# Kernel tuning notes

Measured on AMD Instinct MI355X. Metric: run time of the kernel, lower is better.

## Reference

```python
import jax, jax.numpy as jnp
import numpy as np

D_MODEL = 1024
D_FFN = 2048
N_EXPERTS = 8
TOP_K = 2
B, S = 2, 2048
LN_EPS = 1e-5


def setup_inputs() -> dict:
    key = jax.random.key(0)
    ks = jax.random.split(key, 6)
    scale = 0.02
    x = jax.random.normal(ks[0], (B, S, D_MODEL), dtype=jnp.float32)
    w_router = jax.random.normal(ks[1], (N_EXPERTS, D_MODEL), dtype=jnp.float32) * scale
    w_gate = jax.random.normal(ks[2], (N_EXPERTS, D_FFN, D_MODEL), dtype=jnp.float32) * scale
    w_up = jax.random.normal(ks[3], (N_EXPERTS, D_FFN, D_MODEL), dtype=jnp.float32) * scale
    w_down = jax.random.normal(ks[4], (N_EXPERTS, D_MODEL, D_FFN), dtype=jnp.float32) * scale
    ln_gamma = jnp.ones((D_MODEL,), dtype=jnp.float32)
    ln_beta = jnp.zeros((D_MODEL,), dtype=jnp.float32)
    return {"x": x, "w_router": w_router, "w_gate": w_gate, "w_up": w_up,
            "w_down": w_down, "ln_gamma": ln_gamma, "ln_beta": ln_beta}


def reference(x, w_router, w_gate, w_up, w_down, ln_gamma, ln_beta):
    # Router: top-k logits, softmax over selected k (matches MoERouter)
    logits = jnp.einsum('bsd,ed->bse', x, w_router)            # [B,S,E]
    top_vals, top_idx = jax.lax.top_k(logits, TOP_K)           # [B,S,k]
    rw = jax.nn.softmax(top_vals, axis=-1)                     # [B,S,k]

    # Dense per-expert SwiGLU over ALL tokens (faithful to the looped original:
    # sum over k of mask*weight*expert(x) == gather of per-expert outputs).
    gate = jnp.einsum('bsd,efd->ebsf', x, w_gate)              # [E,B,S,F]
    up = jnp.einsum('bsd,efd->ebsf', x, w_up)                  # [E,B,S,F]
    h = jax.nn.silu(gate) * up                                 # SwiGLU hidden
    y = jnp.einsum('ebsf,edf->bsed', h, w_down)                # [B,S,E,D]

    # Gather the k selected experts per token and combine with routing weights
    sel = jnp.take_along_axis(y, top_idx[..., None], axis=2)   # [B,S,k,D]
    out = jnp.sum(rw[..., None] * sel, axis=2)                 # [B,S,D]

    # LayerNorm (eps=1e-5, elementwise affine)
    mu = jnp.mean(out, axis=-1, keepdims=True)
    var = jnp.mean(jnp.square(out - mu), axis=-1, keepdims=True)
    out = (out - mu) * jax.lax.rsqrt(var + LN_EPS)
    return out * ln_gamma + ln_beta
```

## Files before the change

kernel.cpp:

```cpp
#include <hip/hip_runtime.h>


#define D_MODEL 1024
#define D_FFN   2048
#define N_EXP   8
#define TOKENS  4096
#define LISTCAP 4096
#define ROWS_PAD 8320
#define W_ELEM  16777216u

typedef __bf16 bf16x8 __attribute__((ext_vector_type(8)));
typedef float  f32x4  __attribute__((ext_vector_type(4)));

__device__ __forceinline__ ushort f2bf(float f) {
  union { float f; unsigned u; } v; v.f = f;
  unsigned u = v.u;
  u += 0x7fffu + ((u >> 16) & 1u);
  return (ushort)(u >> 16);
}
__device__ __forceinline__ float bf2f(ushort h) {
  union { unsigned u; float f; } v; v.u = ((unsigned)h) << 16; return v.f;
}
__device__ __forceinline__ void gl2lds16(const ushort* g, ushort* l) {
  __builtin_amdgcn_global_load_lds(
      (const __attribute__((address_space(1))) unsigned int*)g,
      (__attribute__((address_space(3))) unsigned int*)l, 16, 0, 0);
}


__global__ __launch_bounds__(64) void router3_kernel(
    const float* __restrict__ x, const float* __restrict__ wr,
    ushort* __restrict__ xb, int* __restrict__ counts,
    int* __restrict__ tok_list, int* __restrict__ slots, float* __restrict__ wts)
{
  const int token = blockIdx.x;
  const int lane  = threadIdx.x;
  const float* xr = x + (size_t)token * D_MODEL + lane * 16;

  float xv[16];
  #pragma unroll
  for (int j = 0; j < 16; ++j) xv[j] = xr[j];

  ushort* xbr = xb + (size_t)token * D_MODEL + lane * 16;
  #pragma unroll
  for (int half = 0; half < 2; ++half) {
    ushort u8[8];
    #pragma unroll
    for (int j = 0; j < 8; ++j) u8[j] = f2bf(xv[half * 8 + j]);
    *(uint4*)(xbr + half * 8) = *(uint4*)u8;
  }

  float logit[N_EXP];
  #pragma unroll
  for (int e = 0; e < N_EXP; ++e) {
    const float* w = wr + e * D_MODEL + lane * 16;
    float p = 0.f;
    #pragma unroll
    for (int j = 0; j < 16; ++j) p += xv[j] * w[j];
    #pragma unroll
    for (int o = 32; o > 0; o >>= 1) p += __shfl_xor(p, o, 64);
    logit[e] = p;
  }

  if (lane == 0) {
    float v0 = -1e30f, v1 = -1e30f; int i0 = 0, i1 = 0;
    #pragma unroll
    for (int e = 0; e < N_EXP; ++e) {
      float v = logit[e];
      if (v > v0)      { v1 = v0; i1 = i0; v0 = v; i0 = e; }
      else if (v > v1) { v1 = v; i1 = e; }
    }
    float t  = expf(v1 - v0);
    float w0 = 1.f / (1.f + t);
    float w1 = t   / (1.f + t);
    int p0 = atomicAdd(&counts[i0], 1);
    tok_list[i0 * LISTCAP + p0] = token;
    int p1 = atomicAdd(&counts[i1], 1);
    tok_list[i1 * LISTCAP + p1] = token;
    slots[token * 2]     = i0 * LISTCAP + p0;
    slots[token * 2 + 1] = i1 * LISTCAP + p1;
    wts[token * 2]     = w0;
    wts[token * 2 + 1] = w1;
  }
}

__global__ __launch_bounds__(256) void convert3_kernel(
    const float* __restrict__ wg, const float* __restrict__ wu,
    const float* __restrict__ wd, ushort* __restrict__ dstBase)
{
  const int bid = blockIdx.x;
  const int arr = bid >> 13;
  const float* src = (arr == 0) ? wg : (arr == 1) ? wu : wd;
  ushort* dst = dstBase + (size_t)arr * W_ELEM;
  const size_t base = (((size_t)(bid & 8191)) * 256 + threadIdx.x) * 8;
  float4 a = *(const float4*)(src + base);
  float4 b = *(const float4*)(src + base + 4);
  ushort u8[8] = {f2bf(a.x), f2bf(a.y), f2bf(a.z), f2bf(a.w),
                  f2bf(b.x), f2bf(b.y), f2bf(b.z), f2bf(b.w)};
  *(uint4*)(dst + base) = *(uint4*)u8;
}

__global__ __launch_bounds__(256, 3) void gateup3_kernel(
    const ushort* __restrict__ xb, const ushort* __restrict__ WgB,
    const ushort* __restrict__ WuB, const int* __restrict__ counts,
    const int* __restrict__ tok_list, ushort* __restrict__ H)
{
  const int e  = blockIdx.z;
  const int Ne = counts[e];
  const int m0 = blockIdx.y * 128;
  if (m0 >= Ne) return;
  const int n0 = blockIdx.x * 64;

  int rowoff = 0;
  for (int j = 0; j < e; ++j) rowoff += counts[j];

  __shared__ ushort As[128 * 64];
  __shared__ ushort Bg[64 * 64];
  __shared__ ushort Bu[64 * 64];
  __shared__ int tok_s[128];

  const int tid = threadIdx.x;
  if (tid < 128) {
    int i = m0 + tid;
    tok_s[tid] = tok_list[e * LISTCAP + (i < Ne ? i : Ne - 1)];
  }
  __syncthreads();

  const int wave = tid >> 6;
  const int lane = tid & 63;
  const int rsub = lane >> 3;
  const int cchk = lane & 7;
  const int co   = (cchk ^ rsub) << 3;

  const ushort* aSrc[4];
  #pragma unroll
  for (int i = 0; i < 4; ++i)
    aSrc[i] = xb + (size_t)tok_s[wave * 32 + i * 8 + rsub] * D_MODEL + co;
  const ushort* gS = WgB + ((size_t)e * D_FFN + n0 + wave * 16 + rsub) * D_MODEL + co;
  const ushort* uS = WuB + ((size_t)e * D_FFN + n0 + wave * 16 + rsub) * D_MODEL + co;
  ushort* aD = &As[(wave * 32) * 64];
  ushort* gD = &Bg[(wave * 16) * 64];
  ushort* uD = &Bu[(wave * 16) * 64];

  const int wm   = (wave >> 1) * 64;
  const int wn   = (wave & 1) * 32;
  const int lrow = lane & 15;
  const int lq   = lane >> 4;

  f32x4 accg[4][2], accu[4][2];
  #pragma unroll
  for (int i = 0; i < 4; ++i)
    #pragma unroll
    for (int j = 0; j < 2; ++j) {
      accg[i][j] = f32x4{0.f, 0.f, 0.f, 0.f};
      accu[i][j] = f32x4{0.f, 0.f, 0.f, 0.f};
    }

  for (int k0 = 0; k0 < D_MODEL; k0 += 64) {
    #pragma unroll
    for (int i = 0; i < 4; ++i) {
      gl2lds16(aSrc[i], aD + i * 8 * 64);
      aSrc[i] += 64;
    }
    #pragma unroll
    for (int i = 0; i < 2; ++i) {
      gl2lds16(gS + (size_t)i * 8 * D_MODEL, gD + i * 8 * 64);
      gl2lds16(uS + (size_t)i * 8 * D_MODEL, uD + i * 8 * 64);
    }
    gS += 64; uS += 64;
    __syncthreads();

    #pragma unroll
    for (int kk = 0; kk < 2; ++kk) {
      const int c = kk * 4 + lq;
      bf16x8 af[4], bgf[2], buf[2];
      #pragma unroll
      for (int mi = 0; mi < 4; ++mi) {
        int r = wm + mi * 16 + lrow;
        af[mi] = *(const bf16x8*)&As[r * 64 + ((c ^ (r & 7)) << 3)];
      }
      #pragma unroll
      for (int ni = 0; ni < 2; ++ni) {
        int r = wn + ni * 16 + lrow;
        int off = r * 64 + ((c ^ (r & 7)) << 3);
        bgf[ni] = *(const bf16x8*)&Bg[off];
        buf[ni] = *(const bf16x8*)&Bu[off];
      }
      #pragma unroll
      for (int mi = 0; mi < 4; ++mi)
        #pragma unroll
        for (int ni = 0; ni < 2; ++ni) {
          accg[mi][ni] = __builtin_amdgcn_mfma_f32_16x16x32_bf16(af[mi], bgf[ni], accg[mi][ni], 0, 0, 0);
          accu[mi][ni] = __builtin_amdgcn_mfma_f32_16x16x32_bf16(af[mi], buf[ni], accu[mi][ni], 0, 0, 0);
        }
    }
    __syncthreads();
  }

  const int rowbase = rowoff + m0;
  #pragma unroll
  for (int mi = 0; mi < 4; ++mi)
    #pragma unroll
    for (int r4 = 0; r4 < 4; ++r4) {
      int m = wm + mi * 16 + lq * 4 + r4;
      if (m0 + m < Ne) {
        ushort* hr = H + (size_t)(rowbase + m) * D_FFN + n0 + wn + lrow;
        #pragma unroll
        for (int ni = 0; ni < 2; ++ni) {
          float g = accg[mi][ni][r4];
          float u = accu[mi][ni][r4];
          float h = g / (1.f + __expf(-g)) * u;
          hr[ni * 16] = f2bf(h);
        }
      }
    }
}

__global__ __launch_bounds__(256, 3) void down3_kernel(
    const ushort* __restrict__ H, const ushort* __restrict__ WdB,
    const int* __restrict__ counts, ushort* __restrict__ Y)
{
  const int e  = blockIdx.z;
  const int Ne = counts[e];
  const int m0 = blockIdx.y * 128;
  if (m0 >= Ne) return;
  const int n0 = blockIdx.x * 128;

  int rowoff = 0;
  for (int j = 0; j < e; ++j) rowoff += counts[j];
  const int rowbase = rowoff + m0;

  __shared__ ushort As[128 * 64];
  __shared__ ushort Bd[128 * 64];

  const int tid  = threadIdx.x;
  const int wave = tid >> 6;
  const int lane = tid & 63;
  const int rsub = lane >> 3;
  const int cchk = lane & 7;
  const int co   = (cchk ^ rsub) << 3;

  const ushort* aS = H   + (size_t)(rowbase + wave * 32 + rsub) * D_FFN + co;
  const ushort* bS = WdB + (size_t)(e * D_MODEL + n0 + wave * 32 + rsub) * D_FFN + co;
  ushort* aD = &As[(wave * 32) * 64];
  ushort* bD = &Bd[(wave * 32) * 64];

  const int wm   = (wave >> 1) * 64;
  const int wn   = (wave & 1) * 64;
  const int lrow = lane & 15;
  const int lq   = lane >> 4;

  f32x4 acc[4][4];
  #pragma unroll
  for (int i = 0; i < 4; ++i)
    #pragma unroll
    for (int j = 0; j < 4; ++j) acc[i][j] = f32x4{0.f, 0.f, 0.f, 0.f};

  for (int k0 = 0; k0 < D_FFN; k0 += 64) {
    #pragma unroll
    for (int i = 0; i < 4; ++i) {
      gl2lds16(aS + (size_t)i * 8 * D_FFN, aD + i * 8 * 64);
      gl2lds16(bS + (size_t)i * 8 * D_FFN, bD + i * 8 * 64);
    }
    aS += 64; bS += 64;
    __syncthreads();

    #pragma unroll
    for (int kk = 0; kk < 2; ++kk) {
      const int c = kk * 4 + lq;
      bf16x8 af[4], bf[4];
      #pragma unroll
      for (int mi = 0; mi < 4; ++mi) {
        int r = wm + mi * 16 + lrow;
        af[mi] = *(const bf16x8*)&As[r * 64 + ((c ^ (r & 7)) << 3)];
      }
      #pragma unroll
      for (int ni = 0; ni < 4; ++ni) {
        int r = wn + ni * 16 + lrow;
        bf[ni] = *(const bf16x8*)&Bd[r * 64 + ((c ^ (r & 7)) << 3)];
      }
      #pragma unroll
      for (int mi = 0; mi < 4; ++mi)
        #pragma unroll
        for (int ni = 0; ni < 4; ++ni)
          acc[mi][ni] = __builtin_amdgcn_mfma_f32_16x16x32_bf16(af[mi], bf[ni], acc[mi][ni], 0, 0, 0);
    }
    __syncthreads();
  }

  #pragma unroll
  for (int mi = 0; mi < 4; ++mi)
    #pragma unroll
    for (int r4 = 0; r4 < 4; ++r4) {
      int m = wm + mi * 16 + lq * 4 + r4;
      if (m0 + m < Ne) {
        ushort* yr = Y + (size_t)(rowbase + m) * D_MODEL + n0 + wn + lrow;
        #pragma unroll
        for (int ni = 0; ni < 4; ++ni)
          yr[ni * 16] = f2bf(acc[mi][ni][r4]);
      }
    }
}

__global__ __launch_bounds__(256) void combine_ln3_kernel(
    const ushort* __restrict__ Y, const int* __restrict__ slots,
    const float* __restrict__ wts, const int* __restrict__ counts,
    const float* __restrict__ gamma, const float* __restrict__ beta,
    float* __restrict__ out)
{
  const int token = blockIdx.x;
  const int t = threadIdx.x;

  __shared__ int offs_s[N_EXP];
  if (t == 0) {
    int s = 0;
    #pragma unroll
    for (int j = 0; j < N_EXP; ++j) { offs_s[j] = s; s += counts[j]; }
  }
  __syncthreads();

  const int s0 = slots[token * 2], s1 = slots[token * 2 + 1];
  const float w0 = wts[token * 2], w1 = wts[token * 2 + 1];
  const int r0 = offs_s[s0 >> 12] + (s0 & (LISTCAP - 1));
  const int r1 = offs_s[s1 >> 12] + (s1 & (LISTCAP - 1));

  ushort4 a = *(const ushort4*)(Y + (size_t)r0 * D_MODEL + t * 4);
  ushort4 b = *(const ushort4*)(Y + (size_t)r1 * D_MODEL + t * 4);
  float4 v;
  v.x = w0 * bf2f(a.x) + w1 * bf2f(b.x);
  v.y = w0 * bf2f(a.y) + w1 * bf2f(b.y);
  v.z = w0 * bf2f(a.z) + w1 * bf2f(b.z);
  v.w = w0 * bf2f(a.w) + w1 * bf2f(b.w);

  float s = v.x + v.y + v.z + v.w;
  #pragma unroll
  for (int o = 32; o > 0; o >>= 1) s += __shfl_xor(s, o, 64);
  __shared__ float red[4];
  const int wave = t >> 6, lane = t & 63;
  if (lane == 0) red[wave] = s;
  __syncthreads();
  float mean = (red[0] + red[1] + red[2] + red[3]) * (1.f / D_MODEL);

  float dx = v.x - mean, dy = v.y - mean, dz = v.z - mean, dw = v.w - mean;
  float ss = dx * dx + dy * dy + dz * dz + dw * dw;
  #pragma unroll
  for (int o = 32; o > 0; o >>= 1) ss += __shfl_xor(ss, o, 64);
  __syncthreads();
  if (lane == 0) red[wave] = ss;
  __syncthreads();
  float var = (red[0] + red[1] + red[2] + red[3]) * (1.f / D_MODEL);
  float rs  = rsqrtf(var + 1e-5f);

  float4 g = ((const float4*)gamma)[t];
  float4 bb = ((const float4*)beta)[t];
  float4 o4;
  o4.x = dx * rs * g.x + bb.x;
  o4.y = dy * rs * g.y + bb.y;
  o4.z = dz * rs * g.z + bb.z;
  o4.w = dw * rs * g.w + bb.w;
  ((float4*)(out + (size_t)token * D_MODEL))[t] = o4;
}

__global__ __launch_bounds__(64) void router_kernel(
    const float* __restrict__ x, const float* __restrict__ wr,
    ushort* __restrict__ xb, int* __restrict__ counts,
    int* __restrict__ tok_list, float* __restrict__ wt_list)
{
  const int token = blockIdx.x;
  const int lane  = threadIdx.x;
  const float* xr = x + (size_t)token * D_MODEL;
  float xv[16];
  #pragma unroll
  for (int j = 0; j < 16; ++j) xv[j] = xr[j * 64 + lane];
  ushort* xbr = xb + (size_t)token * D_MODEL;
  #pragma unroll
  for (int j = 0; j < 16; ++j) xbr[j * 64 + lane] = f2bf(xv[j]);
  float logit[N_EXP];
  #pragma unroll
  for (int e = 0; e < N_EXP; ++e) {
    const float* w = wr + e * D_MODEL;
    float p = 0.f;
    #pragma unroll
    for (int j = 0; j < 16; ++j) p += xv[j] * w[j * 64 + lane];
    #pragma unroll
    for (int o = 32; o > 0; o >>= 1) p += __shfl_xor(p, o, 64);
    logit[e] = p;
  }
  if (lane == 0) {
    float v0 = -1e30f, v1 = -1e30f; int i0 = 0, i1 = 0;
    #pragma unroll
    for (int e = 0; e < N_EXP; ++e) {
      float v = logit[e];
      if (v > v0)      { v1 = v0; i1 = i0; v0 = v; i0 = e; }
      else if (v > v1) { v1 = v; i1 = e; }
    }
    float t  = expf(v1 - v0);
    float w0 = 1.f / (1.f + t);
    float w1 = t   / (1.f + t);
    int p0 = atomicAdd(&counts[i0], 1);
    tok_list[i0 * LISTCAP + p0] = token;
    wt_list[i0 * LISTCAP + p0] = w0;
    int p1 = atomicAdd(&counts[i1], 1);
    tok_list[i1 * LISTCAP + p1] = token;
    wt_list[i1 * LISTCAP + p1] = w1;
  }
}

__global__ void prefix_kernel(const int* __restrict__ counts, int* __restrict__ offsets)
{
  if (threadIdx.x == 0 && blockIdx.x == 0) {
    int s = 0;
    for (int e = 0; e < N_EXP; ++e) { offsets[e] = s; s += counts[e]; }
  }
}

__global__ __launch_bounds__(256, 2) void gateup_kernel(
    const ushort* __restrict__ xb, const float* __restrict__ wg,
    const float* __restrict__ wu, const int* __restrict__ counts,
    const int* __restrict__ offsets, const int* __restrict__ tok_list,
    ushort* __restrict__ H)
{
  const int e  = blockIdx.z;
  const int Ne = counts[e];
  const int m0 = blockIdx.y * 128;
  if (m0 >= Ne) return;
  const int n0 = blockIdx.x * 128;
  __shared__ ushort As[128][80];
  __shared__ ushort Bg[128][80];
  __shared__ ushort Bu[128][80];
  __shared__ int tok_s[128];
  const int tid = threadIdx.x;
  if (tid < 128) {
    int i = m0 + tid;
    tok_s[tid] = tok_list[e * LISTCAP + (i < Ne ? i : 0)];
  }
  __syncthreads();
  const int wave = tid >> 6;
  const int lane = tid & 63;
  const int wm   = (wave >> 1) * 64;
  const int wn   = (wave & 1) * 64;
  const int lrow = lane & 15;
  const int lk   = (lane >> 4) * 8;
  f32x4 accg[4][4], accu[4][4];
  #pragma unroll
  for (int i = 0; i < 4; ++i)
    #pragma unroll
    for (int j = 0; j < 4; ++j) {
      accg[i][j] = f32x4{0.f, 0.f, 0.f, 0.f};
      accu[i][j] = f32x4{0.f, 0.f, 0.f, 0.f};
    }
  const size_t wbase = ((size_t)e * D_FFN + n0) * D_MODEL;
  for (int k0 = 0; k0 < D_MODEL; k0 += 64) {
    #pragma unroll
    for (int r = 0; r < 4; ++r) {
      int idx = tid + r * 256;
      int row = idx >> 3;
      int c8  = (idx & 7) * 8;
      const ushort* src = xb + (size_t)tok_s[row] * D_MODEL + k0 + c8;
      *(uint4*)(&As[row][c8]) = *(const uint4*)src;
    }
    #pragma unroll
    for (int r = 0; r < 8; ++r) {
      int idx = tid + r * 256;
      int row = idx >> 4;
      int c4  = (idx & 15) * 4;
      const size_t off = wbase + (size_t)row * D_MODEL + k0 + c4;
      const float4 g = *(const float4*)(wg + off);
      const float4 u = *(const float4*)(wu + off);
      ushort4 gb; gb.x = f2bf(g.x); gb.y = f2bf(g.y); gb.z = f2bf(g.z); gb.w = f2bf(g.w);
      ushort4 ub; ub.x = f2bf(u.x); ub.y = f2bf(u.y); ub.z = f2bf(u.z); ub.w = f2bf(u.w);
      *(ushort4*)(&Bg[row][c4]) = gb;
      *(ushort4*)(&Bu[row][c4]) = ub;
    }
    __syncthreads();
    #pragma unroll
    for (int kk = 0; kk < 64; kk += 32) {
      bf16x8 af[4], bgf[4], buf[4];
      #pragma unroll
      for (int mi = 0; mi < 4; ++mi)
        af[mi] = *(const bf16x8*)(&As[wm + mi * 16 + lrow][kk + lk]);
      #pragma unroll
      for (int ni = 0; ni < 4; ++ni) {
        bgf[ni] = *(const bf16x8*)(&Bg[wn + ni * 16 + lrow][kk + lk]);
        buf[ni] = *(const bf16x8*)(&Bu[wn + ni * 16 + lrow][kk + lk]);
      }
      #pragma unroll
      for (int mi = 0; mi < 4; ++mi)
        #pragma unroll
        for (int ni = 0; ni < 4; ++ni) {
          accg[mi][ni] = __builtin_amdgcn_mfma_f32_16x16x32_bf16(af[mi], bgf[ni], accg[mi][ni], 0, 0, 0);
          accu[mi][ni] = __builtin_amdgcn_mfma_f32_16x16x32_bf16(af[mi], buf[ni], accu[mi][ni], 0, 0, 0);
        }
    }
    __syncthreads();
  }
  const int row_base = offsets[e] + m0;
  #pragma unroll
  for (int mi = 0; mi < 4; ++mi)
    #pragma unroll
    for (int ni = 0; ni < 4; ++ni)
      #pragma unroll
      for (int r4 = 0; r4 < 4; ++r4) {
        int m = wm + mi * 16 + (lane >> 4) * 4 + r4;
        if (m0 + m < Ne) {
          int n = wn + ni * 16 + (lane & 15);
          float g = accg[mi][ni][r4];
          float u = accu[mi][ni][r4];
          float h = g / (1.f + __expf(-g)) * u;
          H[(size_t)(row_base + m) * D_FFN + (n0 + n)] = f2bf(h);
        }
      }
}

__global__ __launch_bounds__(256, 2) void down_kernel(
    const ushort* __restrict__ H, const float* __restrict__ wd,
    const int* __restrict__ counts, const int* __restrict__ offsets,
    const int* __restrict__ tok_list, const float* __restrict__ wt_list,
    float* __restrict__ out)
{
  const int e  = blockIdx.z;
  const int Ne = counts[e];
  const int m0 = blockIdx.y * 128;
  if (m0 >= Ne) return;
  const int n0 = blockIdx.x * 128;
  __shared__ ushort As[128][80];
  __shared__ ushort Bd[128][80];
  __shared__ int   tok_s[128];
  __shared__ float wt_s[128];
  const int tid = threadIdx.x;
  if (tid < 128) {
    int i  = m0 + tid;
    int ok = (i < Ne);
    tok_s[tid] = tok_list[e * LISTCAP + (ok ? i : 0)];
    wt_s[tid]  = ok ? wt_list[e * LISTCAP + i] : 0.f;
  }
  __syncthreads();
  const int wave = tid >> 6;
  const int lane = tid & 63;
  const int wm   = (wave >> 1) * 64;
  const int wn   = (wave & 1) * 64;
  const int lrow = lane & 15;
  const int lk   = (lane >> 4) * 8;
  const int row_base = offsets[e] + m0;
  f32x4 acc[4][4];
  #pragma unroll
  for (int i = 0; i < 4; ++i)
    #pragma unroll
    for (int j = 0; j < 4; ++j) acc[i][j] = f32x4{0.f, 0.f, 0.f, 0.f};
  const size_t wdbase = ((size_t)e * D_MODEL + n0) * D_FFN;
  for (int k0 = 0; k0 < D_FFN; k0 += 64) {
    #pragma unroll
    for (int r = 0; r < 4; ++r) {
      int idx = tid + r * 256;
      int row = idx >> 3;
      int c8  = (idx & 7) * 8;
      const ushort* src = H + (size_t)(row_base + row) * D_FFN + k0 + c8;
      *(uint4*)(&As[row][c8]) = *(const uint4*)src;
    }
    #pragma unroll
    for (int r = 0; r < 8; ++r) {
      int idx = tid + r * 256;
      int row = idx >> 4;
      int c4  = (idx & 15) * 4;
      const float4 d = *(const float4*)(wd + wdbase + (size_t)row * D_FFN + k0 + c4);
      ushort4 db; db.x = f2bf(d.x); db.y = f2bf(d.y); db.z = f2bf(d.z); db.w = f2bf(d.w);
      *(ushort4*)(&Bd[row][c4]) = db;
    }
    __syncthreads();
    #pragma unroll
    for (int kk = 0; kk < 64; kk += 32) {
      bf16x8 af[4], bdf[4];
      #pragma unroll
      for (int mi = 0; mi < 4; ++mi)
        af[mi] = *(const bf16x8*)(&As[wm + mi * 16 + lrow][kk + lk]);
      #pragma unroll
      for (int ni = 0; ni < 4; ++ni)
        bdf[ni] = *(const bf16x8*)(&Bd[wn + ni * 16 + lrow][kk + lk]);
      #pragma unroll
      for (int mi = 0; mi < 4; ++mi)
        #pragma unroll
        for (int ni = 0; ni < 4; ++ni)
          acc[mi][ni] = __builtin_amdgcn_mfma_f32_16x16x32_bf16(af[mi], bdf[ni], acc[mi][ni], 0, 0, 0);
    }
    __syncthreads();
  }
  #pragma unroll
  for (int mi = 0; mi < 4; ++mi)
    #pragma unroll
    for (int ni = 0; ni < 4; ++ni)
      #pragma unroll
      for (int r4 = 0; r4 < 4; ++r4) {
        int m = wm + mi * 16 + (lane >> 4) * 4 + r4;
        if (m0 + m < Ne) {
          int n = wn + ni * 16 + (lane & 15);
          float v = acc[mi][ni][r4] * wt_s[m];
          atomicAdd(&out[(size_t)tok_s[m] * D_MODEL + (n0 + n)], v);
        }
      }
}

__global__ __launch_bounds__(256) void ln_kernel(
    float* __restrict__ out, const float* __restrict__ gamma,
    const float* __restrict__ beta)
{
  const int row = blockIdx.x;
  const int t   = threadIdx.x;
  float* rp = out + (size_t)row * D_MODEL;
  float4 v = ((const float4*)rp)[t];
  float s = v.x + v.y + v.z + v.w;
  #pragma unroll
  for (int o = 32; o > 0; o >>= 1) s += __shfl_xor(s, o, 64);
  __shared__ float red[4];
  const int wave = t >> 6, lane = t & 63;
  if (lane == 0) red[wave] = s;
  __syncthreads();
  float mean = (red[0] + red[1] + red[2] + red[3]) * (1.f / D_MODEL);
  float dx = v.x - mean, dy = v.y - mean, dz = v.z - mean, dw = v.w - mean;
  float ss = dx * dx + dy * dy + dz * dz + dw * dw;
  #pragma unroll
  for (int o = 32; o > 0; o >>= 1) ss += __shfl_xor(ss, o, 64);
  __syncthreads();
  if (lane == 0) red[wave] = ss;
  __syncthreads();
  float var = (red[0] + red[1] + red[2] + red[3]) * (1.f / D_MODEL);
  float rs  = rsqrtf(var + 1e-5f);
  float4 g = ((const float4*)gamma)[t];
  float4 b = ((const float4*)beta)[t];
  float4 o4;
  o4.x = dx * rs * g.x + b.x;
  o4.y = dy * rs * g.y + b.y;
  o4.z = dz * rs * g.z + b.z;
  o4.w = dw * rs * g.w + b.w;
  ((float4*)rp)[t] = o4;
}

extern "C" void kernel_launch(void* const* d_in, const int* in_sizes, int n_in,
                              void* d_out, int out_size, void* d_ws, size_t ws_size,
                              hipStream_t stream) {
  const float* x        = (const float*)d_in[0];
  const float* w_router = (const float*)d_in[1];
  const float* w_gate   = (const float*)d_in[2];
  const float* w_up     = (const float*)d_in[3];
  const float* w_down   = (const float*)d_in[4];
  const float* ln_gamma = (const float*)d_in[5];
  const float* ln_beta  = (const float*)d_in[6];
  float* out = (float*)d_out;
  char* ws = (char*)d_ws;

  const size_t META = 262144;
  const size_t NEED = META + 3 * (size_t)W_ELEM * 2
                      + (size_t)TOKENS * D_MODEL * 2
                      + (size_t)ROWS_PAD * D_FFN * 2;

  if (ws_size >= NEED) {
    int*   counts   = (int*)ws;
    int*   tok_list = (int*)(ws + 4096);
    int*   slots    = (int*)(ws + 4096 + 131072);
    float* wts      = (float*)(ws + 4096 + 131072 + 32768);
    ushort* WgB = (ushort*)(ws + META);
    ushort* WuB = WgB + W_ELEM;
    ushort* WdB = WuB + W_ELEM;
    ushort* xb  = WdB + W_ELEM;
    ushort* H   = xb + (size_t)TOKENS * D_MODEL;
    ushort* Y   = WgB;

    hipMemsetAsync(counts, 0, 64, stream);
    router3_kernel<<<TOKENS, 64, 0, stream>>>(x, w_router, xb, counts, tok_list, slots, wts);
    convert3_kernel<<<3 * 8192, 256, 0, stream>>>(w_gate, w_up, w_down, WgB);
    gateup3_kernel<<<dim3(D_FFN / 64, 32, N_EXP), 256, 0, stream>>>(
        xb, WgB, WuB, counts, tok_list, H);
    down3_kernel<<<dim3(D_MODEL / 128, 32, N_EXP), 256, 0, stream>>>(
        H, WdB, counts, Y);
    combine_ln3_kernel<<<TOKENS, 256, 0, stream>>>(Y, slots, wts, counts,
                                                   ln_gamma, ln_beta, out);
  } else {
    int*   counts   = (int*)ws;
    int*   offsets  = counts + 8;
    int*   tok_list = (int*)(ws + 256);
    float* wt_list  = (float*)(ws + 256 + LISTCAP * N_EXP * 4);
    ushort* xb      = (ushort*)(ws + 256 + LISTCAP * N_EXP * 8);
    ushort* H       = xb + (size_t)TOKENS * D_MODEL;

    hipMemsetAsync(counts, 0, 64, stream);
    hipMemsetAsync(out, 0, (size_t)TOKENS * D_MODEL * sizeof(float), stream);
    router_kernel<<<TOKENS, 64, 0, stream>>>(x, w_router, xb, counts, tok_list, wt_list);
    prefix_kernel<<<1, 64, 0, stream>>>(counts, offsets);
    gateup_kernel<<<dim3(D_FFN / 128, 32, N_EXP), 256, 0, stream>>>(
        xb, w_gate, w_up, counts, offsets, tok_list, H);
    down_kernel<<<dim3(D_MODEL / 128, 32, N_EXP), 256, 0, stream>>>(
        H, w_down, counts, offsets, tok_list, wt_list, out);
    ln_kernel<<<TOKENS, 256, 0, stream>>>(out, ln_gamma, ln_beta);
  }
}
```

Measured before the change: 458.0 us.

## Replace atomic routing lists with per-expert prefix-scan list builder

The router now packs four tokens per 256-thread block and writes only each token's two expert ids and weights, with no atomics. A new per-expert kernel builds the token lists and slots deterministically using wave-level shuffle scans plus a block-level prefix, and it also writes the counts, so the memset is dropped. The aim is to remove global atomic contention and make list order deterministic, which may improve locality in the expert GEMMs. The cost is one extra kernel launch.

```diff
diff --git a/kernel.cpp b/kernel.cpp
--- a/kernel.cpp
+++ b/kernel.cpp
@@ -28,13 +28,12 @@
 }
 
 
-__global__ __launch_bounds__(64) void router3_kernel(
+__global__ __launch_bounds__(256) void router_a_kernel(
     const float* __restrict__ x, const float* __restrict__ wr,
-    ushort* __restrict__ xb, int* __restrict__ counts,
-    int* __restrict__ tok_list, int* __restrict__ slots, float* __restrict__ wts)
-{
-  const int token = blockIdx.x;
-  const int lane  = threadIdx.x;
+    ushort* __restrict__ xb, int* __restrict__ eids, float* __restrict__ wts)
+{
+  const int token = blockIdx.x * 4 + (threadIdx.x >> 6);
+  const int lane  = threadIdx.x & 63;
   const float* xr = x + (size_t)token * D_MODEL + lane * 16;
 
   float xv[16];
@@ -71,16 +70,59 @@
       else if (v > v1) { v1 = v; i1 = e; }
     }
     float t  = expf(v1 - v0);
-    float w0 = 1.f / (1.f + t);
-    float w1 = t   / (1.f + t);
-    int p0 = atomicAdd(&counts[i0], 1);
-    tok_list[i0 * LISTCAP + p0] = token;
-    int p1 = atomicAdd(&counts[i1], 1);
-    tok_list[i1 * LISTCAP + p1] = token;
-    slots[token * 2]     = i0 * LISTCAP + p0;
-    slots[token * 2 + 1] = i1 * LISTCAP + p1;
-    wts[token * 2]     = w0;
-    wts[token * 2 + 1] = w1;
+    eids[token] = i0 | (i1 << 8);
+    wts[token * 2]     = 1.f / (1.f + t);
+    wts[token * 2 + 1] = t   / (1.f + t);
+  }
+}
+
+__global__ __launch_bounds__(1024) void build_lists_kernel(
+    const int* __restrict__ eids, int* __restrict__ counts,
+    int* __restrict__ tok_list, int* __restrict__ slots)
+{
+  const int e = blockIdx.x;
+  const int t = threadIdx.x;
+
+  int my_k[4];
+  int c = 0;
+  #pragma unroll
+  for (int i = 0; i < 4; ++i) {
+    int tok = t + i * 1024;
+    int p  = eids[tok];
+    int e0 = p & 0xff, e1 = (p >> 8) & 0xff;
+    my_k[i] = (e0 == e) ? 0 : (e1 == e) ? 1 : -1;
+    c += (my_k[i] >= 0) ? 1 : 0;
+  }
+
+  const int wave = t >> 6, lane = t & 63;
+  int v = c;
+  #pragma unroll
+  for (int o = 1; o < 64; o <<= 1) {
+    int n = __shfl_up(v, o, 64);
+    if (lane >= o) v += n;
+  }
+
+  __shared__ int wsum[16];
+  __shared__ int wbase[16];
+  if (lane == 63) wsum[wave] = v;
+  __syncthreads();
+  if (t == 0) {
+    int s = 0;
+    #pragma unroll
+    for (int w = 0; w < 16; ++w) { wbase[w] = s; s += wsum[w]; }
+    counts[e] = s;
+  }
+  __syncthreads();
+
+  int pos = wbase[wave] + v - c;
+  #pragma unroll
+  for (int i = 0; i < 4; ++i) {
+    int tok = t + i * 1024;
+    if (my_k[i] >= 0) {
+      tok_list[e * LISTCAP + pos] = tok;
+      slots[tok * 2 + my_k[i]] = e * LISTCAP + pos;
+      pos++;
+    }
   }
 }
 
@@ -657,6 +699,7 @@
     int*   tok_list = (int*)(ws + 4096);
     int*   slots    = (int*)(ws + 4096 + 131072);
     float* wts      = (float*)(ws + 4096 + 131072 + 32768);
+    int*   eids     = (int*)(ws + 4096 + 131072 + 32768 + 32768);
     ushort* WgB = (ushort*)(ws + META);
     ushort* WuB = WgB + W_ELEM;
     ushort* WdB = WuB + W_ELEM;
@@ -664,8 +707,8 @@
     ushort* H   = xb + (size_t)TOKENS * D_MODEL;
     ushort* Y   = WgB;
 
-    hipMemsetAsync(counts, 0, 64, stream);
-    router3_kernel<<<TOKENS, 64, 0, stream>>>(x, w_router, xb, counts, tok_list, slots, wts);
+    router_a_kernel<<<TOKENS / 4, 256, 0, stream>>>(x, w_router, xb, eids, wts);
+    build_lists_kernel<<<N_EXP, 1024, 0, stream>>>(eids, counts, tok_list, slots);
     convert3_kernel<<<3 * 8192, 256, 0, stream>>>(w_gate, w_up, w_down, WgB);
     gateup3_kernel<<<dim3(D_FFN / 64, 32, N_EXP), 256, 0, stream>>>(
         xb, WgB, WuB, counts, tok_list, H);
```

After: 375.9 us. -17.9%, faster.
